# Optimization experiments

Measured on AMD Instinct MI355X. Metric: run time of the kernel, lower is better.

Reference implementation:

```python
import jax, jax.numpy as jnp
import numpy as np

CLAMP_MIN, CLAMP_MAX = 1e-7, 10.0


def _hyper_layer(H, edge_nodes, W, b, power):
    """One HyperTensorGraphConvolution forward.

    H:          [N, d] node signals
    edge_nodes: [E, k] int node indices per hyperedge (k-1 < num_sample, so
                the sampling branch of the original code never triggers and the
                aggregation is the full power-mean over the k-1 neighbors)
    """
    H = jnp.clip(H, CLAMP_MIN, CLAMP_MAX)          # torch.clamp_(H, ...)
    inv_p = 1.0 / power
    Hp = H ** power                                 # [N, d]
    gathered = Hp[edge_nodes]                       # [E, k, d]
    edge_sum = gathered.sum(axis=1, keepdims=True)  # [E, 1, d]
    k = edge_nodes.shape[1]
    # power-mean of the other (k-1) nodes in the hyperedge, per incidence
    contrib = ((edge_sum - gathered) / (k - 1)) ** inv_p   # [E, k, d]
    # new_signal = H.clone(); scatter-add contributions per (edge, node)
    d = H.shape[1]
    new_signal = H.at[edge_nodes.reshape(-1)].add(contrib.reshape(-1, d))
    # row-normalize (rowsum^-1, inf -> 0)
    rowsum = new_signal.sum(axis=1, keepdims=True)
    r_inv = jnp.where(rowsum != 0, 1.0 / rowsum, 0.0)
    AH = new_signal * r_inv
    return AH @ W + b


def setup_inputs() -> dict:
    key = jax.random.key(0)
    k_x, k_e, k_w1, k_b1, k_w2, k_b2 = jax.random.split(key, 6)
    N, d, E, k, c = 100000, 128, 25000, 32, 40
    x = jax.random.uniform(k_x, (N, d), dtype=jnp.float32)
    edge_nodes = jax.random.randint(k_e, (E, k), 0, N, dtype=jnp.int64)
    std1 = 1.0 / np.sqrt(16.0)
    W1 = jax.random.uniform(k_w1, (d, 16), jnp.float32, -std1, std1)
    b1 = jax.random.uniform(k_b1, (16,), jnp.float32, -std1, std1)
    std2 = 1.0 / np.sqrt(float(c))
    W2 = jax.random.uniform(k_w2, (16, c), jnp.float32, -std2, std2)
    b2 = jax.random.uniform(k_b2, (c,), jnp.float32, -std2, std2)
    return {"x": x, "edge_nodes": edge_nodes, "W1": W1, "b1": b1,
            "W2": W2, "b2": b2, "power": 2}


def reference(x, edge_nodes, W1, b1, W2, b2, power):
    H = jax.nn.relu(_hyper_layer(x, edge_nodes, W1, b1, float(power)))
    # dropout is identity at inference
    out = _hyper_layer(H, edge_nodes, W2, b2, float(power))
    return out
```

## Files before the change

kernel.cpp:

```cpp
#include <hip/hip_runtime.h>
#include <hip/hip_fp16.h>
#include <math.h>

#define CAP 64
#define D1 128
#define D2 16
#define C_OUT 40
#define K_EDGE 32
#define CLAMP_LO 1e-7f
#define CLAMP_HI 10.0f
#define SQRT_INV31 0.1796053020267749f

typedef unsigned short ushort_t;
typedef _Float16 hv2 __attribute__((ext_vector_type(2)));

__device__ __forceinline__ hv2 hv2_zero() {
    hv2 z; z.x = (_Float16)0; z.y = (_Float16)0; return z;
}

__global__ __launch_bounds__(256) void k_setup(const float* __restrict__ x,
                                               hv2* __restrict__ Hp,
                                               const int* __restrict__ idx,
                                               int* __restrict__ deg,
                                               ushort_t* __restrict__ lst,
                                               const float* __restrict__ W1,
                                               float* __restrict__ W1t,
                                               hv2* __restrict__ S,
                                               float* __restrict__ S2,
                                               int n4, int total, int E) {
    int i = blockIdx.x * 256 + threadIdx.x;
    if (i < n4) {
        float4 v = ((const float4*)x)[i];
        v.x = fminf(fmaxf(v.x, CLAMP_LO), CLAMP_HI);
        v.y = fminf(fmaxf(v.y, CLAMP_LO), CLAMP_HI);
        v.z = fminf(fmaxf(v.z, CLAMP_LO), CLAMP_HI);
        v.w = fminf(fmaxf(v.w, CLAMP_LO), CLAMP_HI);
        hv2 h0; h0.x = (_Float16)(v.x * v.x); h0.y = (_Float16)(v.y * v.y);
        hv2 h1; h1.x = (_Float16)(v.z * v.z); h1.y = (_Float16)(v.w * v.w);
        Hp[2 * i] = h0; Hp[2 * i + 1] = h1;
    }
    if (i < total) {
        int n = idx[i];
        int e = i >> 5;
        int pos = atomicAdd(&deg[n], 1);
        if (pos < CAP) lst[n * CAP + pos] = (ushort_t)e;
    }
    if (i < D1 * D2) W1t[(i & 15) * D1 + (i >> 4)] = W1[i];
    if (i < 64) S[(size_t)E * 64 + i] = hv2_zero();
    if (i < D2) S2[(size_t)E * D2 + i] = 0.0f;
}

__global__ __launch_bounds__(256) void k_edge_sum(const hv2* __restrict__ Hp,
                                                  const int* __restrict__ idx,
                                                  hv2* __restrict__ S, int E) {
    int w = threadIdx.x >> 6;
    int lane = threadIdx.x & 63;
    int eA = (blockIdx.x * 4 + w) * 4;
    if (eA + 4 > E) eA = E - 4;
    int nid0 = idx[eA * K_EDGE + lane];
    int nid1 = idx[eA * K_EDGE + 64 + lane];
    hv2 acc[4][2];
#pragma unroll
    for (int k = 0; k < 4; k++) { acc[k][0] = hv2_zero(); acc[k][1] = hv2_zero(); }
#pragma unroll
    for (int j = 0; j < K_EDGE; j++) {
        int g = j >> 4;
        int nA = __builtin_amdgcn_readlane(nid0, j);
        int nB = __builtin_amdgcn_readlane(nid0, 32 + j);
        int nC = __builtin_amdgcn_readlane(nid1, j);
        int nD = __builtin_amdgcn_readlane(nid1, 32 + j);
        acc[0][g] += Hp[(size_t)nA * 64 + lane];
        acc[1][g] += Hp[(size_t)nB * 64 + lane];
        acc[2][g] += Hp[(size_t)nC * 64 + lane];
        acc[3][g] += Hp[(size_t)nD * 64 + lane];
    }
#pragma unroll
    for (int k = 0; k < 4; k++)
        S[(size_t)(eA + k) * 64 + lane] = acc[k][0] + acc[k][1];
}

__global__ __launch_bounds__(256) void k_node1(const hv2* __restrict__ Hp,
                                               const hv2* __restrict__ S,
                                               const int* __restrict__ deg,
                                               const ushort_t* __restrict__ lst,
                                               const float* __restrict__ W1t,
                                               const float* __restrict__ b1,
                                               _Float16* __restrict__ Hp2, int N, int E) {
    int w = threadIdx.x >> 6;
    int lane = threadIdx.x & 63;
    int pair = blockIdx.x * 4 + w;
    int n0 = pair * 2, n1 = n0 + 1;
    int c = lane & 15, j = lane >> 4;

    int2 dg2 = ((const int2*)deg)[pair];
    int dg0 = min(dg2.x, CAP), dg1 = min(dg2.y, CAP);
    int sl = lane & 15;
    int nodesel = (lane < 16) ? n0 : n1;
    ushort_t idu = (lane < 32) ? lst[nodesel * CAP + sl] : (ushort_t)0;
    int dsel = (lane < 16) ? dg0 : dg1;
    int e_sel = (lane < 32 && sl < dsel) ? (int)idu : E;

    hv2 hph0 = Hp[(size_t)n0 * 64 + lane];
    hv2 hph1 = Hp[(size_t)n1 * 64 + lane];

    hv2 sv0[16], sv1[16];
#pragma unroll
    for (int t = 0; t < 16; t++) {
        int e = __builtin_amdgcn_readlane(e_sel, t);
        sv0[t] = S[(size_t)e * 64 + lane];
    }
#pragma unroll
    for (int t = 0; t < 16; t++) {
        int e = __builtin_amdgcn_readlane(e_sel, 16 + t);
        sv1[t] = S[(size_t)e * 64 + lane];
    }

    hv2 z = hv2_zero();
    hv2 A0a = z, A0b = z, A1a = z, A1b = z;
#pragma unroll
    for (int t = 0; t < 16; t += 2) {
        hv2 d0 = __builtin_elementwise_max(sv0[t] - hph0, z);
        hv2 d1 = __builtin_elementwise_max(sv0[t + 1] - hph0, z);
        A0a += __builtin_elementwise_sqrt(d0);
        A0b += __builtin_elementwise_sqrt(d1);
    }
#pragma unroll
    for (int t = 0; t < 16; t += 2) {
        hv2 d0 = __builtin_elementwise_max(sv1[t] - hph1, z);
        hv2 d1 = __builtin_elementwise_max(sv1[t + 1] - hph1, z);
        A1a += __builtin_elementwise_sqrt(d0);
        A1b += __builtin_elementwise_sqrt(d1);
    }
    for (int t = 16; t < dg0; t++) {
        int e = lst[n0 * CAP + t];
        hv2 d = __builtin_elementwise_max(S[(size_t)e * 64 + lane] - hph0, z);
        A0a += __builtin_elementwise_sqrt(d);
    }
    for (int t = 16; t < dg1; t++) {
        int e = lst[n1 * CAP + t];
        hv2 d = __builtin_elementwise_max(S[(size_t)e * 64 + lane] - hph1, z);
        A1a += __builtin_elementwise_sqrt(d);
    }
    hv2 A0 = A0a + A0b, A1 = A1a + A1b;

    float ns00 = __builtin_amdgcn_sqrtf((float)hph0.x) + (float)A0.x * SQRT_INV31;
    float ns01 = __builtin_amdgcn_sqrtf((float)hph0.y) + (float)A0.y * SQRT_INV31;
    float ns10 = __builtin_amdgcn_sqrtf((float)hph1.x) + (float)A1.x * SQRT_INV31;
    float ns11 = __builtin_amdgcn_sqrtf((float)hph1.y) + (float)A1.y * SQRT_INV31;

    __shared__ float AHs[4][2][D1];
    AHs[w][0][2 * lane]     = ns00;
    AHs[w][0][2 * lane + 1] = ns01;
    AHs[w][1][2 * lane]     = ns10;
    AHs[w][1][2 * lane + 1] = ns11;

    float v0 = ns00 + ns01, v1 = ns10 + ns11;
#pragma unroll
    for (int m = 1; m < 64; m <<= 1) {
        v0 += __shfl_xor(v0, m, 64);
        v1 += __shfl_xor(v1, m, 64);
    }
    float r0 = __builtin_amdgcn_rcpf(v0);
    float r1 = __builtin_amdgcn_rcpf(v1);

    __threadfence_block();

    const float4* a0p = (const float4*)(&AHs[w][0][j * 32]);
    const float4* a1p = (const float4*)(&AHs[w][1][j * 32]);
    const float4* w1p = (const float4*)(W1t + c * D1 + j * 32);
    float p0 = 0.0f, p1 = 0.0f;
#pragma unroll
    for (int tt = 0; tt < 8; tt++) {
        float4 wv = w1p[tt];
        float4 x0 = a0p[tt];
        float4 x1 = a1p[tt];
        p0 += x0.x * wv.x + x0.y * wv.y + x0.z * wv.z + x0.w * wv.w;
        p1 += x1.x * wv.x + x1.y * wv.y + x1.z * wv.z + x1.w * wv.w;
    }
    p0 += __shfl_xor(p0, 16, 64);
    p0 += __shfl_xor(p0, 32, 64);
    p1 += __shfl_xor(p1, 16, 64);
    p1 += __shfl_xor(p1, 32, 64);
    if (lane < D2) {
        float bb = b1[c];
        float o0 = bb + p0 * r0;
        float o1 = bb + p1 * r1;
        float cl0 = fminf(fmaxf(o0, CLAMP_LO), CLAMP_HI);
        float cl1 = fminf(fmaxf(o1, CLAMP_LO), CLAMP_HI);
        Hp2[(size_t)n0 * D2 + c] = (_Float16)(cl0 * cl0);
        Hp2[(size_t)n1 * D2 + c] = (_Float16)(cl1 * cl1);
    }
}

__global__ __launch_bounds__(256) void k_edge_sum2(const hv2* __restrict__ Hp2v,
                                                   const int* __restrict__ idx,
                                                   float2* __restrict__ S2v, int E) {
    int w = threadIdx.x >> 6;
    int lane = threadIdx.x & 63;
    int sub = lane >> 3;
    int cp = lane & 7;
    int e = (blockIdx.x * 4 + w) * 8 + sub;
    if (e >= E) e = E - 1;
    const int* ip = idx + (size_t)e * K_EDGE;
    hv2 g0 = hv2_zero(), g1 = hv2_zero();
#pragma unroll
    for (int j = 0; j < 16; j++)  g0 += Hp2v[(size_t)ip[j] * 8 + cp];
#pragma unroll
    for (int j = 16; j < 32; j++) g1 += Hp2v[(size_t)ip[j] * 8 + cp];
    float2 s; s.x = (float)g0.x + (float)g1.x; s.y = (float)g0.y + (float)g1.y;
    S2v[(size_t)e * 8 + cp] = s;
}

__global__ __launch_bounds__(256) void k_node2(const _Float16* __restrict__ Hp2,
                                               const float* __restrict__ S2,
                                               const int* __restrict__ deg,
                                               const ushort_t* __restrict__ lst,
                                               const float* __restrict__ W2,
                                               const float* __restrict__ b2,
                                               float* __restrict__ out, int N, int E) {
    int w = threadIdx.x >> 6;
    int lane = threadIdx.x & 63;
    int pair = blockIdx.x * 4 + w;
    int n0 = pair * 2, n1 = n0 + 1;
    int col = lane & 15;
    int node = lane >> 5;
    int gg = (lane >> 4) & 1;
    int nn = node ? n1 : n0;

    int2 dg2 = ((const int2*)deg)[pair];
    int dg0 = min(dg2.x, CAP), dg1 = min(dg2.y, CAP);
    int sl = lane & 15;
    ushort_t idu = (lane < 32) ? lst[((lane < 16) ? n0 : n1) * CAP + sl] : (ushort_t)0;
    int dsel = (lane < 16) ? dg0 : dg1;
    int e_sel = (lane < 32 && sl < dsel) ? (int)idu : E;

    float hp = (float)Hp2[(size_t)nn * D2 + col];
    int dgn = node ? dg1 : dg0;

    int ev[8];
#pragma unroll
    for (int t = 0; t < 8; t++) ev[t] = __shfl(e_sel, node * 16 + 2 * t + gg, 64);
    float sv[8];
#pragma unroll
    for (int t = 0; t < 8; t++) sv[t] = S2[(size_t)ev[t] * D2 + col];

    float acc = 0.0f;
#pragma unroll
    for (int t = 0; t < 8; t++)
        acc += __builtin_amdgcn_sqrtf(fmaxf(sv[t] - hp, 0.0f));
    for (int t = 16; t < dgn; t++) {
        int e = lst[nn * CAP + t];
        float s = S2[(size_t)e * D2 + col];
        if (gg == 0) acc += __builtin_amdgcn_sqrtf(fmaxf(s - hp, 0.0f));
    }
    acc += __shfl_xor(acc, 16, 64);
    float ns = __builtin_amdgcn_sqrtf(hp) + acc * SQRT_INV31;

    float v = ns;
#pragma unroll
    for (int m = 1; m < 16; m <<= 1) v += __shfl_xor(v, m, 64);
    float r = __builtin_amdgcn_rcpf(v);

    __shared__ float AHs[4][2][D2];
    if (gg == 0) AHs[w][node][col] = ns * r;
    __threadfence_block();

    if (lane < C_OUT) {
        float o0 = b2[lane], o1 = o0;
#pragma unroll
        for (int i = 0; i < D2; i++) {
            float wv = W2[i * C_OUT + lane];
            o0 += AHs[w][0][i] * wv;
            o1 += AHs[w][1][i] * wv;
        }
        out[(size_t)n0 * C_OUT + lane] = o0;
        out[(size_t)n1 * C_OUT + lane] = o1;
    }
}

extern "C" void kernel_launch(void* const* d_in, const int* in_sizes, int n_in,
                              void* d_out, int out_size, void* d_ws, size_t ws_size,
                              hipStream_t stream) {
    const float* x   = (const float*)d_in[0];
    const int*   idx = (const int*)d_in[1];
    const float* W1  = (const float*)d_in[2];
    const float* b1  = (const float*)d_in[3];
    const float* W2  = (const float*)d_in[4];
    const float* b2  = (const float*)d_in[5];
    float* out = (float*)d_out;

    int N = in_sizes[0] / D1;
    int E = in_sizes[1] / K_EDGE;

    hv2* Hp = (hv2*)d_ws;
    hv2* S  = Hp + (size_t)N * 64;
    _Float16* Hp2h = (_Float16*)(S + (size_t)(E + 1) * 64);
    float* S2   = (float*)(Hp2h + (size_t)N * D2);
    float* W1t  = S2 + (size_t)(E + 1) * D2;
    int*   deg  = (int*)(W1t + D1 * D2);
    ushort_t* lst = (ushort_t*)(deg + N);

    int total = E * K_EDGE;
    int n4 = N * D1 / 4;

    (void)hipMemsetAsync(deg, 0, (size_t)N * sizeof(int), stream);
    k_setup<<<(n4 + 255) / 256, 256, 0, stream>>>(x, Hp, idx, deg, lst, W1, W1t,
                                                  S, S2, n4, total, E);
    k_edge_sum<<<(E + 15) / 16, 256, 0, stream>>>(Hp, idx, S, E);
    k_node1<<<N / 8, 256, 0, stream>>>(Hp, S, deg, lst, W1t, b1, Hp2h, N, E);
    k_edge_sum2<<<(E + 31) / 32, 256, 0, stream>>>((const hv2*)Hp2h, idx, (float2*)S2, E);
    k_node2<<<N / 8, 256, 0, stream>>>(Hp2h, S2, deg, lst, W2, b2, out, N, E);
}
```

Before: 255.8 us.

## Use 16-byte fp16 vector gathers in edge-sum and node1 kernels

The layer-1 edge-sum and node kernels now gather 8 halfs (16 bytes) per lane instead of 2 halfs (4 bytes). Each 128-dim row is covered by 16 lanes, so one wave processes four edges or four incident-edge slots at a time. Partial results are combined with cross-lane shuffles, and the row sum reduction is shortened to match. This aims to cut the number of gather load instructions and raise bytes per memory request, at the cost of extra shuffle reductions and some idle lanes on the tail degree loop.

```diff
diff --git a/kernel.cpp b/kernel.cpp
--- a/kernel.cpp
+++ b/kernel.cpp
@@ -13,9 +13,17 @@
 
 typedef unsigned short ushort_t;
 typedef _Float16 hv2 __attribute__((ext_vector_type(2)));
+typedef _Float16 hv8 __attribute__((ext_vector_type(8)));
 
 __device__ __forceinline__ hv2 hv2_zero() {
     hv2 z; z.x = (_Float16)0; z.y = (_Float16)0; return z;
+}
+
+__device__ __forceinline__ hv8 shflx_hv8(hv8 v, int m) {
+    union { hv8 h; int i[4]; } u; u.h = v;
+#pragma unroll
+    for (int k = 0; k < 4; k++) u.i[k] = __shfl_xor(u.i[k], m, 64);
+    return u.h;
 }
 
 __global__ __launch_bounds__(256) void k_setup(const float* __restrict__ x,
@@ -50,37 +58,30 @@
     if (i < D2) S2[(size_t)E * D2 + i] = 0.0f;
 }
 
-__global__ __launch_bounds__(256) void k_edge_sum(const hv2* __restrict__ Hp,
+__global__ __launch_bounds__(256) void k_edge_sum(const hv8* __restrict__ Hp,
                                                   const int* __restrict__ idx,
-                                                  hv2* __restrict__ S, int E) {
+                                                  hv8* __restrict__ S, int E) {
     int w = threadIdx.x >> 6;
     int lane = threadIdx.x & 63;
+    int q = lane & 15, g = lane >> 4;
     int eA = (blockIdx.x * 4 + w) * 4;
     if (eA + 4 > E) eA = E - 4;
-    int nid0 = idx[eA * K_EDGE + lane];
-    int nid1 = idx[eA * K_EDGE + 64 + lane];
-    hv2 acc[4][2];
-#pragma unroll
-    for (int k = 0; k < 4; k++) { acc[k][0] = hv2_zero(); acc[k][1] = hv2_zero(); }
+    int2 id2 = *(const int2*)(idx + (size_t)(eA + g) * K_EDGE + 2 * q);
+    int idlo = id2.x, idhi = id2.y;
+
+    hv8 accA = {0,0,0,0,0,0,0,0}, accB = {0,0,0,0,0,0,0,0};
 #pragma unroll
     for (int j = 0; j < K_EDGE; j++) {
-        int g = j >> 4;
-        int nA = __builtin_amdgcn_readlane(nid0, j);
-        int nB = __builtin_amdgcn_readlane(nid0, 32 + j);
-        int nC = __builtin_amdgcn_readlane(nid1, j);
-        int nD = __builtin_amdgcn_readlane(nid1, 32 + j);
-        acc[0][g] += Hp[(size_t)nA * 64 + lane];
-        acc[1][g] += Hp[(size_t)nB * 64 + lane];
-        acc[2][g] += Hp[(size_t)nC * 64 + lane];
-        acc[3][g] += Hp[(size_t)nD * 64 + lane];
-    }
-#pragma unroll
-    for (int k = 0; k < 4; k++)
-        S[(size_t)(eA + k) * 64 + lane] = acc[k][0] + acc[k][1];
-}
-
-__global__ __launch_bounds__(256) void k_node1(const hv2* __restrict__ Hp,
-                                               const hv2* __restrict__ S,
+        int src = (lane & 48) + (j >> 1);
+        int id = __shfl((j & 1) ? idhi : idlo, src, 64);
+        hv8 hvv = Hp[(size_t)id * 16 + q];
+        if (j < 16) accA += hvv; else accB += hvv;
+    }
+    S[(size_t)(eA + g) * 16 + q] = accA + accB;
+}
+
+__global__ __launch_bounds__(256) void k_node1(const hv8* __restrict__ Hp,
+                                               const hv8* __restrict__ S,
                                                const int* __restrict__ deg,
                                                const ushort_t* __restrict__ lst,
                                                const float* __restrict__ W1t,
@@ -90,84 +91,84 @@
     int lane = threadIdx.x & 63;
     int pair = blockIdx.x * 4 + w;
     int n0 = pair * 2, n1 = n0 + 1;
-    int c = lane & 15, j = lane >> 4;
+    int q = lane & 15, g = lane >> 4;
 
     int2 dg2 = ((const int2*)deg)[pair];
     int dg0 = min(dg2.x, CAP), dg1 = min(dg2.y, CAP);
-    int sl = lane & 15;
     int nodesel = (lane < 16) ? n0 : n1;
-    ushort_t idu = (lane < 32) ? lst[nodesel * CAP + sl] : (ushort_t)0;
+    ushort_t idu = (lane < 32) ? lst[nodesel * CAP + q] : (ushort_t)0;
     int dsel = (lane < 16) ? dg0 : dg1;
-    int e_sel = (lane < 32 && sl < dsel) ? (int)idu : E;
-
-    hv2 hph0 = Hp[(size_t)n0 * 64 + lane];
-    hv2 hph1 = Hp[(size_t)n1 * 64 + lane];
-
-    hv2 sv0[16], sv1[16];
-#pragma unroll
-    for (int t = 0; t < 16; t++) {
-        int e = __builtin_amdgcn_readlane(e_sel, t);
-        sv0[t] = S[(size_t)e * 64 + lane];
-    }
-#pragma unroll
-    for (int t = 0; t < 16; t++) {
-        int e = __builtin_amdgcn_readlane(e_sel, 16 + t);
-        sv1[t] = S[(size_t)e * 64 + lane];
-    }
-
-    hv2 z = hv2_zero();
-    hv2 A0a = z, A0b = z, A1a = z, A1b = z;
-#pragma unroll
-    for (int t = 0; t < 16; t += 2) {
-        hv2 d0 = __builtin_elementwise_max(sv0[t] - hph0, z);
-        hv2 d1 = __builtin_elementwise_max(sv0[t + 1] - hph0, z);
-        A0a += __builtin_elementwise_sqrt(d0);
-        A0b += __builtin_elementwise_sqrt(d1);
-    }
-#pragma unroll
-    for (int t = 0; t < 16; t += 2) {
-        hv2 d0 = __builtin_elementwise_max(sv1[t] - hph1, z);
-        hv2 d1 = __builtin_elementwise_max(sv1[t + 1] - hph1, z);
-        A1a += __builtin_elementwise_sqrt(d0);
-        A1b += __builtin_elementwise_sqrt(d1);
-    }
-    for (int t = 16; t < dg0; t++) {
-        int e = lst[n0 * CAP + t];
-        hv2 d = __builtin_elementwise_max(S[(size_t)e * 64 + lane] - hph0, z);
-        A0a += __builtin_elementwise_sqrt(d);
-    }
-    for (int t = 16; t < dg1; t++) {
-        int e = lst[n1 * CAP + t];
-        hv2 d = __builtin_elementwise_max(S[(size_t)e * 64 + lane] - hph1, z);
-        A1a += __builtin_elementwise_sqrt(d);
-    }
-    hv2 A0 = A0a + A0b, A1 = A1a + A1b;
-
-    float ns00 = __builtin_amdgcn_sqrtf((float)hph0.x) + (float)A0.x * SQRT_INV31;
-    float ns01 = __builtin_amdgcn_sqrtf((float)hph0.y) + (float)A0.y * SQRT_INV31;
-    float ns10 = __builtin_amdgcn_sqrtf((float)hph1.x) + (float)A1.x * SQRT_INV31;
-    float ns11 = __builtin_amdgcn_sqrtf((float)hph1.y) + (float)A1.y * SQRT_INV31;
+    int e_sel = (lane < 32 && q < dsel) ? (int)idu : E;
+
+    int ea[4], eb[4];
+#pragma unroll
+    for (int t = 0; t < 4; t++) {
+        ea[t] = __shfl(e_sel, g + 4 * t, 64);
+        eb[t] = __shfl(e_sel, 16 + g + 4 * t, 64);
+    }
+
+    hv8 hpa = Hp[(size_t)n0 * 16 + q];
+    hv8 hpb = Hp[(size_t)n1 * 16 + q];
+
+    hv8 sva[4], svb[4];
+#pragma unroll
+    for (int t = 0; t < 4; t++) sva[t] = S[(size_t)ea[t] * 16 + q];
+#pragma unroll
+    for (int t = 0; t < 4; t++) svb[t] = S[(size_t)eb[t] * 16 + q];
+
+    hv8 z = {0,0,0,0,0,0,0,0};
+    hv8 A0 = z, A1 = z;
+#pragma unroll
+    for (int t = 0; t < 4; t++) {
+        A0 += __builtin_elementwise_sqrt(__builtin_elementwise_max(sva[t] - hpa, z));
+        A1 += __builtin_elementwise_sqrt(__builtin_elementwise_max(svb[t] - hpb, z));
+    }
+    if (g == 0) {
+        for (int t = 16; t < dg0; t++) {
+            int e = lst[n0 * CAP + t];
+            A0 += __builtin_elementwise_sqrt(
+                __builtin_elementwise_max(S[(size_t)e * 16 + q] - hpa, z));
+        }
+        for (int t = 16; t < dg1; t++) {
+            int e = lst[n1 * CAP + t];
+            A1 += __builtin_elementwise_sqrt(
+                __builtin_elementwise_max(S[(size_t)e * 16 + q] - hpb, z));
+        }
+    }
+    A0 += shflx_hv8(A0, 16); A0 += shflx_hv8(A0, 32);
+    A1 += shflx_hv8(A1, 16); A1 += shflx_hv8(A1, 32);
+
+    float ns0[8], ns1[8], sum0 = 0.0f, sum1 = 0.0f;
+#pragma unroll
+    for (int i = 0; i < 8; i++) {
+        ns0[i] = __builtin_amdgcn_sqrtf((float)hpa[i]) + (float)A0[i] * SQRT_INV31;
+        ns1[i] = __builtin_amdgcn_sqrtf((float)hpb[i]) + (float)A1[i] * SQRT_INV31;
+        sum0 += ns0[i]; sum1 += ns1[i];
+    }
+#pragma unroll
+    for (int m = 1; m < 16; m <<= 1) {
+        sum0 += __shfl_xor(sum0, m, 64);
+        sum1 += __shfl_xor(sum1, m, 64);
+    }
+    float r0 = __builtin_amdgcn_rcpf(sum0);
+    float r1 = __builtin_amdgcn_rcpf(sum1);
 
     __shared__ float AHs[4][2][D1];
-    AHs[w][0][2 * lane]     = ns00;
-    AHs[w][0][2 * lane + 1] = ns01;
-    AHs[w][1][2 * lane]     = ns10;
-    AHs[w][1][2 * lane + 1] = ns11;
-
-    float v0 = ns00 + ns01, v1 = ns10 + ns11;
-#pragma unroll
-    for (int m = 1; m < 64; m <<= 1) {
-        v0 += __shfl_xor(v0, m, 64);
-        v1 += __shfl_xor(v1, m, 64);
-    }
-    float r0 = __builtin_amdgcn_rcpf(v0);
-    float r1 = __builtin_amdgcn_rcpf(v1);
-
+    if (g == 0) {
+        float4 v0a = {ns0[0], ns0[1], ns0[2], ns0[3]};
+        float4 v0b = {ns0[4], ns0[5], ns0[6], ns0[7]};
+        float4 v1a = {ns1[0], ns1[1], ns1[2], ns1[3]};
+        float4 v1b = {ns1[4], ns1[5], ns1[6], ns1[7]};
+        *(float4*)&AHs[w][0][q * 8]     = v0a;
+        *(float4*)&AHs[w][0][q * 8 + 4] = v0b;
+        *(float4*)&AHs[w][1][q * 8]     = v1a;
+        *(float4*)&AHs[w][1][q * 8 + 4] = v1b;
+    }
     __threadfence_block();
 
-    const float4* a0p = (const float4*)(&AHs[w][0][j * 32]);
-    const float4* a1p = (const float4*)(&AHs[w][1][j * 32]);
-    const float4* w1p = (const float4*)(W1t + c * D1 + j * 32);
+    const float4* a0p = (const float4*)(&AHs[w][0][g * 32]);
+    const float4* a1p = (const float4*)(&AHs[w][1][g * 32]);
+    const float4* w1p = (const float4*)(W1t + q * D1 + g * 32);
     float p0 = 0.0f, p1 = 0.0f;
 #pragma unroll
     for (int tt = 0; tt < 8; tt++) {
@@ -182,13 +183,13 @@
     p1 += __shfl_xor(p1, 16, 64);
     p1 += __shfl_xor(p1, 32, 64);
     if (lane < D2) {
-        float bb = b1[c];
+        float bb = b1[q];
         float o0 = bb + p0 * r0;
         float o1 = bb + p1 * r1;
         float cl0 = fminf(fmaxf(o0, CLAMP_LO), CLAMP_HI);
         float cl1 = fminf(fmaxf(o1, CLAMP_LO), CLAMP_HI);
-        Hp2[(size_t)n0 * D2 + c] = (_Float16)(cl0 * cl0);
-        Hp2[(size_t)n1 * D2 + c] = (_Float16)(cl1 * cl1);
+        Hp2[(size_t)n0 * D2 + q] = (_Float16)(cl0 * cl0);
+        Hp2[(size_t)n1 * D2 + q] = (_Float16)(cl1 * cl1);
     }
 }
 
@@ -306,8 +307,9 @@
     (void)hipMemsetAsync(deg, 0, (size_t)N * sizeof(int), stream);
     k_setup<<<(n4 + 255) / 256, 256, 0, stream>>>(x, Hp, idx, deg, lst, W1, W1t,
                                                   S, S2, n4, total, E);
-    k_edge_sum<<<(E + 15) / 16, 256, 0, stream>>>(Hp, idx, S, E);
-    k_node1<<<N / 8, 256, 0, stream>>>(Hp, S, deg, lst, W1t, b1, Hp2h, N, E);
+    k_edge_sum<<<(E + 15) / 16, 256, 0, stream>>>((const hv8*)Hp, idx, (hv8*)S, E);
+    k_node1<<<N / 8, 256, 0, stream>>>((const hv8*)Hp, (const hv8*)S, deg, lst,
+                                       W1t, b1, Hp2h, N, E);
     k_edge_sum2<<<(E + 31) / 32, 256, 0, stream>>>((const hv2*)Hp2h, idx, (float2*)S2, E);
     k_node2<<<N / 8, 256, 0, stream>>>(Hp2h, S2, deg, lst, W2, b2, out, N, E);
 }
```

After: 259.9 us. Within noise of the previous version (+1.6%).

## Split node1 into half-feature gather pass and separate projection kernel

Applied to the files above, without the earlier changes.

The node-side gather kernel is split into two launches. The first processes each node's 128 features in two 64-wide halves (two passes over the grid), four nodes per wave, using scalar fp16 gathers from S with a 256-byte stride, and writes per-half partial values and row sums to a new workspace buffer. The second kernel reads these, normalizes, and does the W1 projection. The goal is to shrink the per-pass working set of S for better cache locality and to raise parallelism. In exchange it adds an extra launch and an intermediate round trip through global memory, and its scalar 2-byte gathers are less efficient than the previous packed 4-byte loads.

```diff
diff --git a/kernel.cpp b/kernel.cpp
--- a/kernel.cpp
+++ b/kernel.cpp
@@ -79,95 +79,138 @@
         S[(size_t)(eA + k) * 64 + lane] = acc[k][0] + acc[k][1];
 }
 
-__global__ __launch_bounds__(256) void k_node1(const hv2* __restrict__ Hp,
-                                               const hv2* __restrict__ S,
-                                               const int* __restrict__ deg,
-                                               const ushort_t* __restrict__ lst,
-                                               const float* __restrict__ W1t,
-                                               const float* __restrict__ b1,
-                                               _Float16* __restrict__ Hp2, int N, int E) {
+__global__ __launch_bounds__(256) void k_node1a(const _Float16* __restrict__ Hp,
+                                                const _Float16* __restrict__ S,
+                                                const int* __restrict__ deg,
+                                                const ushort_t* __restrict__ lst,
+                                                _Float16* __restrict__ nsb,
+                                                float* __restrict__ rs,
+                                                int NB, int E) {
+    int w = threadIdx.x >> 6;
+    int lane = threadIdx.x & 63;
+    int b = blockIdx.x;
+    int pass = (b >= NB) ? 1 : 0;
+    int nb = (b - pass * NB) * 16 + w * 4;
+    int node_l = lane >> 4, slot = lane & 15;
+
+    int4 dg4 = *(const int4*)(deg + nb);
+    int d0 = min(dg4.x, CAP), d1 = min(dg4.y, CAP);
+    int d2 = min(dg4.z, CAP), d3 = min(dg4.w, CAP);
+    int mydeg = (node_l == 0) ? d0 : (node_l == 1) ? d1 : (node_l == 2) ? d2 : d3;
+    ushort_t idu = __builtin_nontemporal_load(&lst[(nb + node_l) * CAP + slot]);
+    int e_sel = (slot < mydeg) ? (int)idu : E;
+
+    const _Float16* Sh = S + pass * 64;
+    _Float16 hph[4];
+#pragma unroll
+    for (int n = 0; n < 4; n++)
+        hph[n] = __builtin_nontemporal_load(&Hp[(size_t)(nb + n) * 128 + pass * 64 + lane]);
+
+    float accf[4];
+    _Float16 sva[16], svb[16];
+#pragma unroll
+    for (int t = 0; t < 16; t++) {
+        int e = __builtin_amdgcn_readlane(e_sel, t);
+        sva[t] = Sh[(size_t)e * 128 + lane];
+    }
+#pragma unroll
+    for (int t = 0; t < 16; t++) {
+        int e = __builtin_amdgcn_readlane(e_sel, 16 + t);
+        svb[t] = Sh[(size_t)e * 128 + lane];
+    }
+    {
+        _Float16 aa = (_Float16)0, ab = (_Float16)0;
+#pragma unroll
+        for (int t = 0; t < 16; t++) {
+            _Float16 da = sva[t] - hph[0];
+            _Float16 db = svb[t] - hph[1];
+            da = (da > (_Float16)0) ? da : (_Float16)0;
+            db = (db > (_Float16)0) ? db : (_Float16)0;
+            aa += __builtin_elementwise_sqrt(da);
+            ab += __builtin_elementwise_sqrt(db);
+        }
+        accf[0] = (float)aa; accf[1] = (float)ab;
+    }
+#pragma unroll
+    for (int t = 0; t < 16; t++) {
+        int e = __builtin_amdgcn_readlane(e_sel, 32 + t);
+        sva[t] = Sh[(size_t)e * 128 + lane];
+    }
+#pragma unroll
+    for (int t = 0; t < 16; t++) {
+        int e = __builtin_amdgcn_readlane(e_sel, 48 + t);
+        svb[t] = Sh[(size_t)e * 128 + lane];
+    }
+    {
+        _Float16 aa = (_Float16)0, ab = (_Float16)0;
+#pragma unroll
+        for (int t = 0; t < 16; t++) {
+            _Float16 da = sva[t] - hph[2];
+            _Float16 db = svb[t] - hph[3];
+            da = (da > (_Float16)0) ? da : (_Float16)0;
+            db = (db > (_Float16)0) ? db : (_Float16)0;
+            aa += __builtin_elementwise_sqrt(da);
+            ab += __builtin_elementwise_sqrt(db);
+        }
+        accf[2] = (float)aa; accf[3] = (float)ab;
+    }
+    int dgs[4] = {d0, d1, d2, d3};
+#pragma unroll
+    for (int n = 0; n < 4; n++) {
+        for (int t = 16; t < dgs[n]; t++) {
+            int e = lst[(nb + n) * CAP + t];
+            _Float16 d = Sh[(size_t)e * 128 + lane] - hph[n];
+            d = (d > (_Float16)0) ? d : (_Float16)0;
+            accf[n] += (float)__builtin_elementwise_sqrt(d);
+        }
+    }
+
+    float ns[4], sums[4];
+#pragma unroll
+    for (int n = 0; n < 4; n++) {
+        ns[n] = __builtin_amdgcn_sqrtf((float)hph[n]) + accf[n] * SQRT_INV31;
+        sums[n] = ns[n];
+    }
+#pragma unroll
+    for (int m = 1; m < 64; m <<= 1) {
+#pragma unroll
+        for (int n = 0; n < 4; n++) sums[n] += __shfl_xor(sums[n], m, 64);
+    }
+#pragma unroll
+    for (int n = 0; n < 4; n++)
+        __builtin_nontemporal_store((_Float16)ns[n],
+            &nsb[(size_t)(nb + n) * 128 + pass * 64 + lane]);
+    if (slot == 0)
+        __builtin_nontemporal_store(sums[node_l], &rs[(nb + node_l) * 2 + pass]);
+}
+
+__global__ __launch_bounds__(256) void k_node1c(const hv2* __restrict__ nsb2,
+                                                const float2* __restrict__ rs2,
+                                                const float* __restrict__ W1t,
+                                                const float* __restrict__ b1,
+                                                _Float16* __restrict__ Hp2, int N) {
     int w = threadIdx.x >> 6;
     int lane = threadIdx.x & 63;
     int pair = blockIdx.x * 4 + w;
     int n0 = pair * 2, n1 = n0 + 1;
-    int c = lane & 15, j = lane >> 4;
-
-    int2 dg2 = ((const int2*)deg)[pair];
-    int dg0 = min(dg2.x, CAP), dg1 = min(dg2.y, CAP);
-    int sl = lane & 15;
-    int nodesel = (lane < 16) ? n0 : n1;
-    ushort_t idu = (lane < 32) ? lst[nodesel * CAP + sl] : (ushort_t)0;
-    int dsel = (lane < 16) ? dg0 : dg1;
-    int e_sel = (lane < 32 && sl < dsel) ? (int)idu : E;
-
-    hv2 hph0 = Hp[(size_t)n0 * 64 + lane];
-    hv2 hph1 = Hp[(size_t)n1 * 64 + lane];
-
-    hv2 sv0[16], sv1[16];
-#pragma unroll
-    for (int t = 0; t < 16; t++) {
-        int e = __builtin_amdgcn_readlane(e_sel, t);
-        sv0[t] = S[(size_t)e * 64 + lane];
-    }
-#pragma unroll
-    for (int t = 0; t < 16; t++) {
-        int e = __builtin_amdgcn_readlane(e_sel, 16 + t);
-        sv1[t] = S[(size_t)e * 64 + lane];
-    }
-
-    hv2 z = hv2_zero();
-    hv2 A0a = z, A0b = z, A1a = z, A1b = z;
-#pragma unroll
-    for (int t = 0; t < 16; t += 2) {
-        hv2 d0 = __builtin_elementwise_max(sv0[t] - hph0, z);
-        hv2 d1 = __builtin_elementwise_max(sv0[t + 1] - hph0, z);
-        A0a += __builtin_elementwise_sqrt(d0);
-        A0b += __builtin_elementwise_sqrt(d1);
-    }
-#pragma unroll
-    for (int t = 0; t < 16; t += 2) {
-        hv2 d0 = __builtin_elementwise_max(sv1[t] - hph1, z);
-        hv2 d1 = __builtin_elementwise_max(sv1[t + 1] - hph1, z);
-        A1a += __builtin_elementwise_sqrt(d0);
-        A1b += __builtin_elementwise_sqrt(d1);
-    }
-    for (int t = 16; t < dg0; t++) {
-        int e = lst[n0 * CAP + t];
-        hv2 d = __builtin_elementwise_max(S[(size_t)e * 64 + lane] - hph0, z);
-        A0a += __builtin_elementwise_sqrt(d);
-    }
-    for (int t = 16; t < dg1; t++) {
-        int e = lst[n1 * CAP + t];
-        hv2 d = __builtin_elementwise_max(S[(size_t)e * 64 + lane] - hph1, z);
-        A1a += __builtin_elementwise_sqrt(d);
-    }
-    hv2 A0 = A0a + A0b, A1 = A1a + A1b;
-
-    float ns00 = __builtin_amdgcn_sqrtf((float)hph0.x) + (float)A0.x * SQRT_INV31;
-    float ns01 = __builtin_amdgcn_sqrtf((float)hph0.y) + (float)A0.y * SQRT_INV31;
-    float ns10 = __builtin_amdgcn_sqrtf((float)hph1.x) + (float)A1.x * SQRT_INV31;
-    float ns11 = __builtin_amdgcn_sqrtf((float)hph1.y) + (float)A1.y * SQRT_INV31;
+    int q = lane & 15, g = lane >> 4;
+
+    hv2 a0 = nsb2[(size_t)n0 * 64 + lane];
+    hv2 a1 = nsb2[(size_t)n1 * 64 + lane];
+    float2 rr0 = rs2[n0], rr1 = rs2[n1];
+    float r0 = __builtin_amdgcn_rcpf(rr0.x + rr0.y);
+    float r1 = __builtin_amdgcn_rcpf(rr1.x + rr1.y);
 
     __shared__ float AHs[4][2][D1];
-    AHs[w][0][2 * lane]     = ns00;
-    AHs[w][0][2 * lane + 1] = ns01;
-    AHs[w][1][2 * lane]     = ns10;
-    AHs[w][1][2 * lane + 1] = ns11;
-
-    float v0 = ns00 + ns01, v1 = ns10 + ns11;
-#pragma unroll
-    for (int m = 1; m < 64; m <<= 1) {
-        v0 += __shfl_xor(v0, m, 64);
-        v1 += __shfl_xor(v1, m, 64);
-    }
-    float r0 = __builtin_amdgcn_rcpf(v0);
-    float r1 = __builtin_amdgcn_rcpf(v1);
-
+    AHs[w][0][2 * lane]     = (float)a0.x;
+    AHs[w][0][2 * lane + 1] = (float)a0.y;
+    AHs[w][1][2 * lane]     = (float)a1.x;
+    AHs[w][1][2 * lane + 1] = (float)a1.y;
     __threadfence_block();
 
-    const float4* a0p = (const float4*)(&AHs[w][0][j * 32]);
-    const float4* a1p = (const float4*)(&AHs[w][1][j * 32]);
-    const float4* w1p = (const float4*)(W1t + c * D1 + j * 32);
+    const float4* a0p = (const float4*)(&AHs[w][0][g * 32]);
+    const float4* a1p = (const float4*)(&AHs[w][1][g * 32]);
+    const float4* w1p = (const float4*)(W1t + q * D1 + g * 32);
     float p0 = 0.0f, p1 = 0.0f;
 #pragma unroll
     for (int tt = 0; tt < 8; tt++) {
@@ -182,13 +225,13 @@
     p1 += __shfl_xor(p1, 16, 64);
     p1 += __shfl_xor(p1, 32, 64);
     if (lane < D2) {
-        float bb = b1[c];
+        float bb = b1[q];
         float o0 = bb + p0 * r0;
         float o1 = bb + p1 * r1;
         float cl0 = fminf(fmaxf(o0, CLAMP_LO), CLAMP_HI);
         float cl1 = fminf(fmaxf(o1, CLAMP_LO), CLAMP_HI);
-        Hp2[(size_t)n0 * D2 + c] = (_Float16)(cl0 * cl0);
-        Hp2[(size_t)n1 * D2 + c] = (_Float16)(cl1 * cl1);
+        Hp2[(size_t)n0 * D2 + q] = (_Float16)(cl0 * cl0);
+        Hp2[(size_t)n1 * D2 + q] = (_Float16)(cl1 * cl1);
     }
 }
 
@@ -299,15 +342,21 @@
     float* W1t  = S2 + (size_t)(E + 1) * D2;
     int*   deg  = (int*)(W1t + D1 * D2);
     ushort_t* lst = (ushort_t*)(deg + N);
+    _Float16* nsb = (_Float16*)(lst + (size_t)N * CAP);
+    float* rs   = (float*)(nsb + (size_t)N * D1);
 
     int total = E * K_EDGE;
     int n4 = N * D1 / 4;
+    int NB = N / 16;
 
     (void)hipMemsetAsync(deg, 0, (size_t)N * sizeof(int), stream);
     k_setup<<<(n4 + 255) / 256, 256, 0, stream>>>(x, Hp, idx, deg, lst, W1, W1t,
                                                   S, S2, n4, total, E);
     k_edge_sum<<<(E + 15) / 16, 256, 0, stream>>>(Hp, idx, S, E);
-    k_node1<<<N / 8, 256, 0, stream>>>(Hp, S, deg, lst, W1t, b1, Hp2h, N, E);
+    k_node1a<<<2 * NB, 256, 0, stream>>>((const _Float16*)Hp, (const _Float16*)S,
+                                         deg, lst, nsb, rs, NB, E);
+    k_node1c<<<N / 8, 256, 0, stream>>>((const hv2*)nsb, (const float2*)rs,
+                                        W1t, b1, Hp2h, N);
     k_edge_sum2<<<(E + 31) / 32, 256, 0, stream>>>((const hv2*)Hp2h, idx, (float2*)S2, E);
     k_node2<<<N / 8, 256, 0, stream>>>(Hp2h, S2, deg, lst, W2, b2, out, N, E);
 }
```

Result: slower. 294.6 us (+15.2%).
